# Kernel optimization log

Measured on AMD Instinct MI355X. Metric: run time of the kernel, lower is better.

The kernel has to match this reference:

```python
import jax, jax.numpy as jnp
import numpy as np

DFAUD = 1024
DFRGB = 1024
DIM_K = 1024
N_HEADS = 4
B, T = 16, 1024


def setup_inputs() -> dict:
    key = jax.random.key(0)
    ks = jax.random.split(key, 11)
    s = lambda d: 1.0 / np.sqrt(d)
    return {
        "x": jax.random.normal(ks[0], (B, T, DFAUD), jnp.float32),
        "y": jax.random.normal(ks[1], (B, T, DFRGB), jnp.float32),
        "adj": jax.random.normal(ks[2], (B, T, T), jnp.float32),
        "Wq": jax.random.uniform(ks[3], (DIM_K, DFAUD), jnp.float32, -s(DFAUD), s(DFAUD)),
        "bq": jnp.zeros((DIM_K,), jnp.float32),
        "Wk": jax.random.uniform(ks[4], (DIM_K, DFRGB), jnp.float32, -s(DFRGB), s(DFRGB)),
        "bk": jnp.zeros((DIM_K,), jnp.float32),
        "Wv": jax.random.uniform(ks[5], (DIM_K, DFRGB), jnp.float32, -s(DFRGB), s(DFRGB)),
        "bv": jnp.zeros((DIM_K,), jnp.float32),
        "Wo": jax.random.uniform(ks[6], (DFRGB, DIM_K), jnp.float32, -s(DIM_K), s(DIM_K)),
        "bo": jnp.zeros((DFRGB,), jnp.float32),
    }


def reference(x, y, adj, Wq, bq, Wk, bk, Wv, bv, Wo, bo):
    b, t = x.shape[0], x.shape[1]
    dh = DIM_K // N_HEADS
    norm = 1.0 / np.sqrt(DIM_K)
    # Faithful reproduction of the torch reshape(-1, B, T, dim_k // n_heads):
    # [B, T, dim_k] -> [n_heads, B, T, dh] (row-major reshape, layout-mixing for h>1)
    Q = (x @ Wq.T + bq).reshape(N_HEADS, b, t, dh)
    K = (y @ Wk.T + bk).reshape(N_HEADS, b, t, dh)
    V = (y @ Wv.T + bv).reshape(N_HEADS, b, t, dh)
    scores = jnp.einsum('hbqd,hbkd->hbqk', Q, K) * norm  # [h, B, T, T]
    att = jax.nn.softmax(scores + adj, axis=-1)          # adj [B,T,T] broadcasts
    temp = jnp.einsum('hbqk,hbkd->hbqd', att, V).reshape(b, t, DIM_K)
    out = (temp @ Wo.T + bo).reshape(-1, t, y.shape[2])
    return out
```

## Files before the change

kernel.cpp:

```cpp
#include <hip/hip_runtime.h>
#include <stdint.h>
#include <string.h>

typedef unsigned short u16;
typedef __attribute__((ext_vector_type(8))) short short8_t;
typedef __attribute__((ext_vector_type(4))) float f32x4;

typedef const __attribute__((address_space(1))) void GV;
typedef __attribute__((address_space(3))) void LV;

__device__ __forceinline__ void gload_lds16(const void* g, void* l) {
  __builtin_amdgcn_global_load_lds((GV*)g, (LV*)l, 16, 0, 0);
}

__device__ __forceinline__ u16 f2bf(float f) {
  union { float f; uint32_t u; } v; v.f = f;
  return (u16)((v.u + 0x7FFFu + ((v.u >> 16) & 1u)) >> 16);
}

__device__ __forceinline__ f32x4 fz4() { f32x4 v = {0.f, 0.f, 0.f, 0.f}; return v; }

__global__ __launch_bounds__(256) void cast2_kernel(const float* __restrict__ in0,
                                                    const float* __restrict__ in1,
                                                    u16* __restrict__ out0,
                                                    u16* __restrict__ out1) {
  const int half = blockIdx.x >> 14;
  const float* in = half ? in1 : in0;
  u16* out = half ? out1 : out0;
  int i = ((blockIdx.x & 16383) * 256 + threadIdx.x) * 4;
  float4 v = *(const float4*)(in + i);
  ushort4 o;
  o.x = f2bf(v.x); o.y = f2bf(v.y); o.z = f2bf(v.z); o.w = f2bf(v.w);
  *(ushort4*)(out + i) = o;
}

__global__ __launch_bounds__(256) void cast4_kernel(const float* __restrict__ w0,
                                                    const float* __restrict__ w1,
                                                    const float* __restrict__ w2,
                                                    const float* __restrict__ w3,
                                                    u16* __restrict__ o0,
                                                    u16* __restrict__ o1,
                                                    u16* __restrict__ o2,
                                                    u16* __restrict__ o3) {
  const int sel = blockIdx.x >> 10;
  const float* in = sel == 0 ? w0 : sel == 1 ? w1 : sel == 2 ? w2 : w3;
  u16* out = sel == 0 ? o0 : sel == 1 ? o1 : sel == 2 ? o2 : o3;
  int i = ((blockIdx.x & 1023) * 256 + threadIdx.x) * 4;
  float4 v = *(const float4*)(in + i);
  ushort4 o;
  o.x = f2bf(v.x); o.y = f2bf(v.y); o.z = f2bf(v.z); o.w = f2bf(v.w);
  *(ushort4*)(out + i) = o;
}

__device__ __forceinline__ void gemm8_core(int bid, const u16* __restrict__ A,
                                           const u16* __restrict__ B,
                                           const float* __restrict__ bias,
                                           void* __restrict__ Cout, int mode,
                                           u16* Al, u16* Bl) {
  const int M = 16384, N = 1024, K = 1024;
  (void)M;
  const int tid = threadIdx.x, w = tid >> 6, l = tid & 63;
  const int g = l >> 4, q = l & 15;
  const int xcd = bid & 7;
  const int nt = (bid >> 3) & 3;
  const int mt = xcd * 8 + (bid >> 5);
  const int n0 = nt * 256, m0 = mt * 256;
  const int NT = K >> 6;
  const int ah = w >> 2;
  const int bh = (w & 3) >> 1;
  const int brow0 = ((w & 3) & 1) * 64;

#define STAGE_A(S, half)                                                          \
  {                                                                               \
    _Pragma("unroll") for (int j_ = 0; j_ < 2; ++j_) {                            \
      const int idx_ = j_ * 512 + tid;                                            \
      const int row_ = idx_ >> 3;                                                 \
      const int sl_ = (idx_ & 7) ^ (((idx_ >> 5) & 1) << 1);                      \
      gload_lds16(A + (size_t)(m0 + (half) * 128 + row_) * K + (S) * 64 + sl_ * 8,\
                  Al + ((S) & 1) * 16384 + (half) * 8192 + (j_ * 512 + w * 64) * 8);\
    }                                                                             \
  }
#define STAGE_B(S, half)                                                          \
  {                                                                               \
    _Pragma("unroll") for (int j_ = 0; j_ < 2; ++j_) {                            \
      const int idx_ = j_ * 512 + tid;                                            \
      const int row_ = idx_ >> 3;                                                 \
      const int sl_ = (idx_ & 7) ^ (((idx_ >> 5) & 1) << 1);                      \
      gload_lds16(B + (size_t)(n0 + (half) * 128 + row_) * K + (S) * 64 + sl_ * 8,\
                  Bl + ((S) & 1) * 16384 + (half) * 8192 + (j_ * 512 + w * 64) * 8);\
    }                                                                             \
  }

  f32x4 acc[8][4];
#pragma unroll
  for (int i = 0; i < 8; ++i)
#pragma unroll
    for (int n = 0; n < 4; ++n) acc[i][n] = fz4();

  float bv[4];
#pragma unroll
  for (int nf = 0; nf < 4; ++nf) bv[nf] = bias[n0 + (w & 3) * 64 + nf * 16 + q];

  STAGE_A(0, 0); STAGE_A(0, 1); STAGE_B(0, 0); STAGE_B(0, 1);
  STAGE_A(1, 0); STAGE_A(1, 1); STAGE_B(1, 0); STAGE_B(1, 1);
  asm volatile("s_waitcnt vmcnt(8)");
  __builtin_amdgcn_s_barrier();

  short8_t bfr[4][2];
  for (int S = 0; S < NT; ++S) {
    const int bs = (S & 1) * 16384;
#pragma unroll
    for (int p = 0; p < 4; ++p) {
      short8_t afr[2][2];
#pragma unroll
      for (int mi = 0; mi < 2; ++mi)
#pragma unroll
        for (int kk = 0; kk < 2; ++kk) {
          const int r = (2 * p + mi) * 16 + q;
          afr[mi][kk] = *(const short8_t*)(Al + bs + ah * 8192 + r * 64 +
                                           ((kk * 4 + g) ^ (((r >> 2) & 1) << 1)) * 8);
        }
      if (p == 0) {
#pragma unroll
        for (int nf = 0; nf < 4; ++nf)
#pragma unroll
          for (int kk = 0; kk < 2; ++kk) {
            const int r = brow0 + nf * 16 + q;
            bfr[nf][kk] = *(const short8_t*)(Bl + bs + bh * 8192 + r * 64 +
                                             ((kk * 4 + g) ^ (((r >> 2) & 1) << 1)) * 8);
          }
      }
      if (p == 0 && S >= 1 && S + 1 < NT) STAGE_A(S + 1, 0);
      if (p == 1 && S >= 1 && S + 1 < NT) STAGE_A(S + 1, 1);
      if (p == 2 && S + 2 < NT) STAGE_B(S + 2, 0);
      if (p == 3 && S + 2 < NT) STAGE_B(S + 2, 1);
      if (p == 3) {
        if (S == NT - 2) { asm volatile("s_waitcnt vmcnt(0)"); }
        else if (S < NT - 2) { asm volatile("s_waitcnt vmcnt(4)"); }
      }
      __builtin_amdgcn_s_barrier();
      asm volatile("s_waitcnt lgkmcnt(0)" ::: "memory");
      __builtin_amdgcn_sched_barrier(0);
      __builtin_amdgcn_s_setprio(1);
#pragma unroll
      for (int nf = 0; nf < 4; ++nf)
#pragma unroll
        for (int mi = 0; mi < 2; ++mi)
#pragma unroll
          for (int kk = 0; kk < 2; ++kk)
            acc[2 * p + mi][nf] = __builtin_amdgcn_mfma_f32_16x16x32_bf16(
                afr[mi][kk], bfr[nf][kk], acc[2 * p + mi][nf], 0, 0, 0);
      __builtin_amdgcn_s_setprio(0);
      __builtin_amdgcn_s_barrier();
    }
  }
#undef STAGE_A
#undef STAGE_B

  const int wr = (w >> 2) * 128, wc = (w & 3) * 64;
#pragma unroll
  for (int nf = 0; nf < 4; ++nf) {
    const int col = n0 + wc + nf * 16 + q;
#pragma unroll
    for (int mf = 0; mf < 8; ++mf) {
      const int rowb = m0 + wr + mf * 16 + g * 4;
#pragma unroll
      for (int j = 0; j < 4; ++j) {
        const float vv = acc[mf][nf][j] + bv[nf];
        const int row = rowb + j;
        if (mode == 0) {
          ((float*)Cout)[(size_t)row * N + col] = vv;
        } else if (mode == 1) {
          ((u16*)Cout)[(size_t)row * N + col] = f2bf(vv);
        } else {
          ((u16*)Cout)[((size_t)(row >> 8) << 18) + ((size_t)(col & 255) << 10) +
                       ((row & 255) * 4) + (col >> 8)] = f2bf(vv);
        }
      }
    }
  }
}

__global__ __launch_bounds__(512, 2) void gemm8_qkv(const u16* __restrict__ Xb,
                                                    const u16* __restrict__ Yb,
                                                    const u16* __restrict__ Wqb,
                                                    const u16* __restrict__ Wkb,
                                                    const u16* __restrict__ Wvb,
                                                    const float* __restrict__ bq,
                                                    const float* __restrict__ bk,
                                                    const float* __restrict__ bv,
                                                    u16* __restrict__ Qb,
                                                    u16* __restrict__ Kb,
                                                    u16* __restrict__ VTb) {
  __shared__ u16 Al[2 * 16384];
  __shared__ u16 Bl[2 * 16384];
  const int sel = blockIdx.x >> 8, bid = blockIdx.x & 255;
  const u16* A;
  const u16* B;
  const float* bias;
  void* C;
  int mode;
  if (sel == 0)      { A = Xb; B = Wqb; bias = bq; C = Qb;  mode = 1; }
  else if (sel == 1) { A = Yb; B = Wkb; bias = bk; C = Kb;  mode = 1; }
  else               { A = Yb; B = Wvb; bias = bv; C = VTb; mode = 2; }
  gemm8_core(bid, A, B, bias, C, mode, Al, Bl);
}

__global__ __launch_bounds__(512, 2) void gemm8_out(const u16* __restrict__ A,
                                                    const u16* __restrict__ B,
                                                    const float* __restrict__ bias,
                                                    float* __restrict__ C) {
  __shared__ u16 Al[2 * 16384];
  __shared__ u16 Bl[2 * 16384];
  gemm8_core(blockIdx.x, A, B, bias, C, 0, Al, Bl);
}

__global__ __launch_bounds__(256) void attn_kernel(const u16* __restrict__ Q,
                                                   const u16* __restrict__ Kf,
                                                   const u16* __restrict__ VT,
                                                   const float* __restrict__ adj,
                                                   u16* __restrict__ O) {
  __shared__ u16 Ks[32 * 256];
  __shared__ u16 Vs[256 * 32];
  const int tid = threadIdx.x, w = tid >> 6, l = tid & 63;
  const int g = l >> 4, q = l & 15;
  const int bid = blockIdx.x;
  const int xcd = bid & 7, idx = bid >> 3;
  const int b = xcd * 2 + (idx >> 6);
  const int qb = (idx >> 2) & 15, h = idx & 3;
  const int hb = h * 16 + b;
  const int q0 = qb * 64;
  const u16* qb_p = Q + ((size_t)hb * 1024 + q0 + w * 16) * 256;
  const u16* kb = Kf + (size_t)hb * 1024 * 256;
  const u16* vtb = VT + (size_t)hb * 256 * 1024;
  const float* adjr = adj + (size_t)b * 1024 * 1024 + (size_t)(q0 + w * 16 + q) * 1024;

  const int krow_b = tid >> 5;
  const int kslot = tid & 31;
  const int vdr_b = tid >> 2;
  const int vsl = tid & 3;

  short8_t qf[8];
#pragma unroll
  for (int kk = 0; kk < 8; ++kk)
    qf[kk] = *(const short8_t*)(qb_p + (size_t)q * 256 + kk * 32 + g * 8);

  f32x4 o[16];
#pragma unroll
  for (int n = 0; n < 16; ++n) o[n] = fz4();
  float mrun = -1e30f, lrun = 0.f;

  short8_t kst[4], vst[4];

#define LOADREGS(ktt)                                                              \
  {                                                                                \
    _Pragma("unroll") for (int i_ = 0; i_ < 4; ++i_) {                             \
      const int row_ = i_ * 8 + krow_b;                                            \
      kst[i_] = *(const short8_t*)(kb + (size_t)((ktt) * 32 + row_) * 256 +        \
                                   kslot * 8);                                     \
    }                                                                              \
    _Pragma("unroll") for (int i_ = 0; i_ < 4; ++i_) {                             \
      const int dr_ = i_ * 64 + vdr_b;                                             \
      vst[i_] = *(const short8_t*)(vtb + (size_t)dr_ * 1024 + (ktt) * 32 +         \
                                   vsl * 8);                                       \
    }                                                                              \
  }
#define WRITEREGS()                                                                \
  {                                                                                \
    _Pragma("unroll") for (int i_ = 0; i_ < 4; ++i_) {                             \
      const int row_ = i_ * 8 + krow_b;                                            \
      *(short8_t*)((char*)Ks + row_ * 512 + ((kslot ^ (row_ & 7)) * 16)) = kst[i_];\
    }                                                                              \
    _Pragma("unroll") for (int i_ = 0; i_ < 4; ++i_) {                             \
      const int dr_ = i_ * 64 + vdr_b;                                             \
      *(short8_t*)((char*)Vs + dr_ * 64 + ((vsl ^ ((dr_ >> 1) & 3)) * 16)) = vst[i_];\
    }                                                                              \
  }

  LOADREGS(0);
  float4 a0 = *(const float4*)(adjr + 0 * 32 + 0 * 16 + g * 4);
  float4 a1 = *(const float4*)(adjr + 0 * 32 + 1 * 16 + g * 4);
  WRITEREGS();
  __syncthreads();

  for (int kt = 0; kt < 32; ++kt) {
    float4 n0v = a0, n1v = a1;
    if (kt < 31) {
      LOADREGS(kt + 1);
      n0v = *(const float4*)(adjr + (kt + 1) * 32 + 0 * 16 + g * 4);
      n1v = *(const float4*)(adjr + (kt + 1) * 32 + 1 * 16 + g * 4);
    }

    f32x4 s[2];
    __builtin_amdgcn_s_setprio(1);
#pragma unroll
    for (int f = 0; f < 2; ++f) {
      f32x4 a = fz4();
      const int row = f * 16 + q;
      const char* kr = (const char*)Ks + row * 512;
#pragma unroll
      for (int kk = 0; kk < 8; ++kk) {
        const int cb = kk * 64 + g * 16;
        short8_t kfr = *(const short8_t*)(kr + (cb ^ ((row & 7) << 4)));
        a = __builtin_amdgcn_mfma_f32_16x16x32_bf16(kfr, qf[kk], a, 0, 0, 0);
      }
      s[f] = a;
    }
    __builtin_amdgcn_s_setprio(0);

#pragma unroll
    for (int j = 0; j < 4; ++j) {
      s[0][j] = s[0][j] * 0.03125f + ((const float*)&a0)[j];
      s[1][j] = s[1][j] * 0.03125f + ((const float*)&a1)[j];
    }

    float pmax = s[0][0];
#pragma unroll
    for (int j = 1; j < 4; ++j) pmax = fmaxf(pmax, s[0][j]);
#pragma unroll
    for (int j = 0; j < 4; ++j) pmax = fmaxf(pmax, s[1][j]);
    pmax = fmaxf(pmax, __shfl_xor(pmax, 16));
    pmax = fmaxf(pmax, __shfl_xor(pmax, 32));

    if (!__all(pmax - mrun <= 8.0f)) {
      const float mn = fmaxf(mrun, pmax);
      const float al = __expf(mrun - mn);
      mrun = mn;
      lrun *= al;
#pragma unroll
      for (int n = 0; n < 16; ++n)
#pragma unroll
        for (int r = 0; r < 4; ++r) o[n][r] *= al;
    }

    float sum = 0.f;
#pragma unroll
    for (int f = 0; f < 2; ++f)
#pragma unroll
      for (int j = 0; j < 4; ++j) {
        const float p = __expf(s[f][j] - mrun);
        s[f][j] = p;
        sum += p;
      }
    sum += __shfl_xor(sum, 16);
    sum += __shfl_xor(sum, 32);
    lrun += sum;

    uint32_t W00, W01, W10, W11;
    asm("v_cvt_pk_bf16_f32 %0, %1, %2" : "=v"(W00) : "v"(s[0][0]), "v"(s[0][1]));
    asm("v_cvt_pk_bf16_f32 %0, %1, %2" : "=v"(W01) : "v"(s[0][2]), "v"(s[0][3]));
    asm("v_cvt_pk_bf16_f32 %0, %1, %2" : "=v"(W10) : "v"(s[1][0]), "v"(s[1][1]));
    asm("v_cvt_pk_bf16_f32 %0, %1, %2" : "=v"(W11) : "v"(s[1][2]), "v"(s[1][3]));
    const uint32_t sA0 = (g < 2) ? W00 : W10;
    const uint32_t sA1 = (g < 2) ? W01 : W11;
    const uint32_t sB0 = (g < 2) ? W10 : W00;
    const uint32_t sB1 = (g < 2) ? W11 : W01;
    const uint32_t A0 = (uint32_t)__shfl_xor((int)sA0, 16);
    const uint32_t A1 = (uint32_t)__shfl_xor((int)sA1, 16);
    const uint32_t B0 = (uint32_t)__shfl_xor((int)sB0, 32);
    const uint32_t B1 = (uint32_t)__shfl_xor((int)sB1, 32);
    const uint32_t C0 = (uint32_t)__shfl_xor((int)sB0, 48);
    const uint32_t C1 = (uint32_t)__shfl_xor((int)sB1, 48);
    union { uint32_t u[4]; short8_t v; } pu;
    pu.u[0] = (g == 0) ? W00 : (g == 1) ? C0 : (g == 2) ? B0 : A0;
    pu.u[1] = (g == 0) ? W01 : (g == 1) ? C1 : (g == 2) ? B1 : A1;
    pu.u[2] = (g == 0) ? A0 : (g == 1) ? B0 : (g == 2) ? C0 : W10;
    pu.u[3] = (g == 0) ? A1 : (g == 1) ? B1 : (g == 2) ? C1 : W11;
    const short8_t pa = pu.v;

    __builtin_amdgcn_s_setprio(1);
#pragma unroll
    for (int n = 0; n < 16; ++n) {
      const int dr = n * 16 + q;
      const int sl = g ^ ((dr >> 1) & 3);
      short8_t vf = *(const short8_t*)((const char*)Vs + dr * 64 + sl * 16);
      o[n] = __builtin_amdgcn_mfma_f32_16x16x32_bf16(vf, pa, o[n], 0, 0, 0);
    }
    __builtin_amdgcn_s_setprio(0);

    if (kt < 31) {
      __syncthreads();
      WRITEREGS();
      __syncthreads();
    }
    a0 = n0v; a1 = n1v;
  }
#undef LOADREGS
#undef WRITEREGS

  const float inv = 1.0f / lrun;
  u16* ob = O + ((size_t)hb * 1024 + q0 + w * 16 + q) * 256;
#pragma unroll
  for (int n = 0; n < 16; ++n) {
    ushort4 st;
    st.x = f2bf(o[n][0] * inv); st.y = f2bf(o[n][1] * inv);
    st.z = f2bf(o[n][2] * inv); st.w = f2bf(o[n][3] * inv);
    *(ushort4*)(ob + n * 16 + g * 4) = st;
  }
}

extern "C" void kernel_launch(void* const* d_in, const int* in_sizes, int n_in,
                              void* d_out, int out_size, void* d_ws, size_t ws_size,
                              hipStream_t stream) {
  (void)in_sizes; (void)n_in; (void)out_size; (void)ws_size;
  const float* x   = (const float*)d_in[0];
  const float* y   = (const float*)d_in[1];
  const float* adj = (const float*)d_in[2];
  const float* Wq  = (const float*)d_in[3];
  const float* bq  = (const float*)d_in[4];
  const float* Wk  = (const float*)d_in[5];
  const float* bk  = (const float*)d_in[6];
  const float* Wv  = (const float*)d_in[7];
  const float* bv  = (const float*)d_in[8];
  const float* Wo  = (const float*)d_in[9];
  const float* bo  = (const float*)d_in[10];

  char* ws = (char*)d_ws;
  const size_t MB = 1ull << 20;
  u16* Xb  = (u16*)(ws + 0);
  u16* Yb  = (u16*)(ws + 32 * MB);
  u16* Wqb = (u16*)(ws + 64 * MB);
  u16* Wkb = (u16*)(ws + 66 * MB);
  u16* Wvb = (u16*)(ws + 68 * MB);
  u16* Wob = (u16*)(ws + 70 * MB);
  u16* Qb  = (u16*)(ws + 72 * MB);
  u16* Kb  = (u16*)(ws + 104 * MB);
  u16* VTb = (u16*)(ws + 168 * MB);
  u16* Tmp = Xb;

  cast2_kernel<<<32768, 256, 0, stream>>>(x, y, Xb, Yb);
  cast4_kernel<<<4096, 256, 0, stream>>>(Wq, Wk, Wv, Wo, Wqb, Wkb, Wvb, Wob);

  gemm8_qkv<<<768, 512, 0, stream>>>(Xb, Yb, Wqb, Wkb, Wvb, bq, bk, bv, Qb, Kb, VTb);

  attn_kernel<<<1024, 256, 0, stream>>>(Qb, Kb, VTb, adj, Tmp);

  gemm8_out<<<256, 512, 0, stream>>>(Tmp, Wob, bo, (float*)d_out);
}
```

Measured before the change: 380.0 us.

## Permute weight rows so GEMM epilogues emit vectorized 4-wide stores; merge cast kernels

Each B-tile row is remapped through a permutation so every lane's four MFMA column fragments land on contiguous output columns. The epilogue can then write ushort4 or float4 instead of scalar stores, including for the transposed V layout. The mode is also made a template parameter, and the two cast kernels are merged into one launch. The cost is more complex row-index math in the B loads and bias fetch, and correctness depends on the permutation matching the store layout.

Result: faster. 332.3 us (-12.6%).

```diff
diff --git a/kernel.cpp b/kernel.cpp
--- a/kernel.cpp
+++ b/kernel.cpp
@@ -20,45 +20,46 @@
 
 __device__ __forceinline__ f32x4 fz4() { f32x4 v = {0.f, 0.f, 0.f, 0.f}; return v; }
 
-__global__ __launch_bounds__(256) void cast2_kernel(const float* __restrict__ in0,
-                                                    const float* __restrict__ in1,
-                                                    u16* __restrict__ out0,
-                                                    u16* __restrict__ out1) {
-  const int half = blockIdx.x >> 14;
-  const float* in = half ? in1 : in0;
-  u16* out = half ? out1 : out0;
-  int i = ((blockIdx.x & 16383) * 256 + threadIdx.x) * 4;
+__global__ __launch_bounds__(256) void cast_all(const float* __restrict__ x,
+                                                const float* __restrict__ y,
+                                                const float* __restrict__ w0,
+                                                const float* __restrict__ w1,
+                                                const float* __restrict__ w2,
+                                                const float* __restrict__ w3,
+                                                u16* __restrict__ xo,
+                                                u16* __restrict__ yo,
+                                                u16* __restrict__ o0,
+                                                u16* __restrict__ o1,
+                                                u16* __restrict__ o2,
+                                                u16* __restrict__ o3) {
+  const int bid = blockIdx.x;
+  const float* in;
+  u16* out;
+  int off;
+  if (bid < 32768) {
+    in = (bid < 16384) ? x : y;
+    out = (bid < 16384) ? xo : yo;
+    off = bid & 16383;
+  } else {
+    const int s = (bid - 32768) >> 10;
+    in = s == 0 ? w0 : s == 1 ? w1 : s == 2 ? w2 : w3;
+    out = s == 0 ? o0 : s == 1 ? o1 : s == 2 ? o2 : o3;
+    off = (bid - 32768) & 1023;
+  }
+  int i = (off * 256 + threadIdx.x) * 4;
   float4 v = *(const float4*)(in + i);
   ushort4 o;
   o.x = f2bf(v.x); o.y = f2bf(v.y); o.z = f2bf(v.z); o.w = f2bf(v.w);
   *(ushort4*)(out + i) = o;
 }
 
-__global__ __launch_bounds__(256) void cast4_kernel(const float* __restrict__ w0,
-                                                    const float* __restrict__ w1,
-                                                    const float* __restrict__ w2,
-                                                    const float* __restrict__ w3,
-                                                    u16* __restrict__ o0,
-                                                    u16* __restrict__ o1,
-                                                    u16* __restrict__ o2,
-                                                    u16* __restrict__ o3) {
-  const int sel = blockIdx.x >> 10;
-  const float* in = sel == 0 ? w0 : sel == 1 ? w1 : sel == 2 ? w2 : w3;
-  u16* out = sel == 0 ? o0 : sel == 1 ? o1 : sel == 2 ? o2 : o3;
-  int i = ((blockIdx.x & 1023) * 256 + threadIdx.x) * 4;
-  float4 v = *(const float4*)(in + i);
-  ushort4 o;
-  o.x = f2bf(v.x); o.y = f2bf(v.y); o.z = f2bf(v.z); o.w = f2bf(v.w);
-  *(ushort4*)(out + i) = o;
-}
-
+template <int MODE>
 __device__ __forceinline__ void gemm8_core(int bid, const u16* __restrict__ A,
                                            const u16* __restrict__ B,
                                            const float* __restrict__ bias,
-                                           void* __restrict__ Cout, int mode,
+                                           void* __restrict__ Cout,
                                            u16* Al, u16* Bl) {
-  const int M = 16384, N = 1024, K = 1024;
-  (void)M;
+  const int N = 1024, K = 1024;
   const int tid = threadIdx.x, w = tid >> 6, l = tid & 63;
   const int g = l >> 4, q = l & 15;
   const int xcd = bid & 7;
@@ -70,6 +71,10 @@
   const int bh = (w & 3) >> 1;
   const int brow0 = ((w & 3) & 1) * 64;
 
+#define BROW(u)                                                                   \
+  (MODE == 2 ? ((((u) >> 4) & 3) * 256 + nt * 64 + (((u) >> 6) & 3) * 16 + ((u) & 15)) \
+             : (n0 + (((u) & 0xC0) | (((u) & 15) << 2) | (((u) >> 4) & 3))))
+
 #define STAGE_A(S, half)                                                          \
   {                                                                               \
     _Pragma("unroll") for (int j_ = 0; j_ < 2; ++j_) {                            \
@@ -86,7 +91,8 @@
       const int idx_ = j_ * 512 + tid;                                            \
       const int row_ = idx_ >> 3;                                                 \
       const int sl_ = (idx_ & 7) ^ (((idx_ >> 5) & 1) << 1);                      \
-      gload_lds16(B + (size_t)(n0 + (half) * 128 + row_) * K + (S) * 64 + sl_ * 8,\
+      const int pr_ = BROW((half) * 128 + row_);                                  \
+      gload_lds16(B + (size_t)pr_ * K + (S) * 64 + sl_ * 8,                       \
                   Bl + ((S) & 1) * 16384 + (half) * 8192 + (j_ * 512 + w * 64) * 8);\
     }                                                                             \
   }
@@ -97,9 +103,10 @@
 #pragma unroll
     for (int n = 0; n < 4; ++n) acc[i][n] = fz4();
 
+  const int wc = (w & 3) * 64;
   float bv[4];
 #pragma unroll
-  for (int nf = 0; nf < 4; ++nf) bv[nf] = bias[n0 + (w & 3) * 64 + nf * 16 + q];
+  for (int nf = 0; nf < 4; ++nf) bv[nf] = bias[BROW(wc + nf * 16 + q)];
 
   STAGE_A(0, 0); STAGE_A(0, 1); STAGE_B(0, 0); STAGE_B(0, 1);
   STAGE_A(1, 0); STAGE_A(1, 1); STAGE_B(1, 0); STAGE_B(1, 1);
@@ -156,25 +163,46 @@
   }
 #undef STAGE_A
 #undef STAGE_B
-
-  const int wr = (w >> 2) * 128, wc = (w & 3) * 64;
-#pragma unroll
-  for (int nf = 0; nf < 4; ++nf) {
-    const int col = n0 + wc + nf * 16 + q;
+#undef BROW
+
+  const int wr = (w >> 2) * 128;
+  if (MODE == 2) {
+    const int dvt = nt * 64 + (w & 3) * 16 + q;
 #pragma unroll
     for (int mf = 0; mf < 8; ++mf) {
-      const int rowb = m0 + wr + mf * 16 + g * 4;
 #pragma unroll
       for (int j = 0; j < 4; ++j) {
-        const float vv = acc[mf][nf][j] + bv[nf];
-        const int row = rowb + j;
-        if (mode == 0) {
-          ((float*)Cout)[(size_t)row * N + col] = vv;
-        } else if (mode == 1) {
-          ((u16*)Cout)[(size_t)row * N + col] = f2bf(vv);
+        const int row = m0 + wr + mf * 16 + g * 4 + j;
+        ushort4 st;
+        st.x = f2bf(acc[mf][0][j] + bv[0]);
+        st.y = f2bf(acc[mf][1][j] + bv[1]);
+        st.z = f2bf(acc[mf][2][j] + bv[2]);
+        st.w = f2bf(acc[mf][3][j] + bv[3]);
+        *(ushort4*)((u16*)Cout + (((size_t)(row >> 8)) << 18) +
+                    (((size_t)dvt) << 10) + ((row & 255) << 2)) = st;
+      }
+    }
+  } else {
+    const int colb = n0 + wc + q * 4;
+#pragma unroll
+    for (int mf = 0; mf < 8; ++mf) {
+#pragma unroll
+      for (int j = 0; j < 4; ++j) {
+        const int row = m0 + wr + mf * 16 + g * 4 + j;
+        if (MODE == 0) {
+          float4 fv;
+          fv.x = acc[mf][0][j] + bv[0];
+          fv.y = acc[mf][1][j] + bv[1];
+          fv.z = acc[mf][2][j] + bv[2];
+          fv.w = acc[mf][3][j] + bv[3];
+          *(float4*)((float*)Cout + (size_t)row * N + colb) = fv;
         } else {
-          ((u16*)Cout)[((size_t)(row >> 8) << 18) + ((size_t)(col & 255) << 10) +
-                       ((row & 255) * 4) + (col >> 8)] = f2bf(vv);
+          ushort4 st;
+          st.x = f2bf(acc[mf][0][j] + bv[0]);
+          st.y = f2bf(acc[mf][1][j] + bv[1]);
+          st.z = f2bf(acc[mf][2][j] + bv[2]);
+          st.w = f2bf(acc[mf][3][j] + bv[3]);
+          *(ushort4*)((u16*)Cout + (size_t)row * N + colb) = st;
         }
       }
     }
@@ -195,15 +223,9 @@
   __shared__ u16 Al[2 * 16384];
   __shared__ u16 Bl[2 * 16384];
   const int sel = blockIdx.x >> 8, bid = blockIdx.x & 255;
-  const u16* A;
-  const u16* B;
-  const float* bias;
-  void* C;
-  int mode;
-  if (sel == 0)      { A = Xb; B = Wqb; bias = bq; C = Qb;  mode = 1; }
-  else if (sel == 1) { A = Yb; B = Wkb; bias = bk; C = Kb;  mode = 1; }
-  else               { A = Yb; B = Wvb; bias = bv; C = VTb; mode = 2; }
-  gemm8_core(bid, A, B, bias, C, mode, Al, Bl);
+  if (sel == 0)      gemm8_core<1>(bid, Xb, Wqb, bq, Qb, Al, Bl);
+  else if (sel == 1) gemm8_core<1>(bid, Yb, Wkb, bk, Kb, Al, Bl);
+  else               gemm8_core<2>(bid, Yb, Wvb, bv, VTb, Al, Bl);
 }
 
 __global__ __launch_bounds__(512, 2) void gemm8_out(const u16* __restrict__ A,
@@ -212,7 +234,7 @@
                                                     float* __restrict__ C) {
   __shared__ u16 Al[2 * 16384];
   __shared__ u16 Bl[2 * 16384];
-  gemm8_core(blockIdx.x, A, B, bias, C, 0, Al, Bl);
+  gemm8_core<0>(blockIdx.x, A, B, bias, C, Al, Bl);
 }
 
 __global__ __launch_bounds__(256) void attn_kernel(const u16* __restrict__ Q,
@@ -428,8 +450,8 @@
   u16* VTb = (u16*)(ws + 168 * MB);
   u16* Tmp = Xb;
 
-  cast2_kernel<<<32768, 256, 0, stream>>>(x, y, Xb, Yb);
-  cast4_kernel<<<4096, 256, 0, stream>>>(Wq, Wk, Wv, Wo, Wqb, Wkb, Wvb, Wob);
+  cast_all<<<36864, 256, 0, stream>>>(x, y, Wq, Wk, Wv, Wo,
+                                      Xb, Yb, Wqb, Wkb, Wvb, Wob);
 
   gemm8_qkv<<<768, 512, 0, stream>>>(Xb, Yb, Wqb, Wkb, Wvb, bq, bk, bv, Qb, Kb, VTb);
 
```
